# Performance work log

Hardware: AMD Instinct MI355X
Metric: run time of the kernel (lower is better)

Reference implementation:

```python
import jax, jax.numpy as jnp
import numpy as np

N, F_IN, HEADS, D_HEAD, NCLASS = 4096, 512, 8, 8, 16
NEG_INF = -9e15
LEAKY_SLOPE = 0.2


def setup_inputs() -> dict:
    key = jax.random.key(0)
    ks = jax.random.split(key, 8)
    x = jax.random.normal(ks[0], (N, F_IN), dtype=jnp.float32)
    adj = (jax.random.uniform(ks[1], (N, N)) < 0.01).astype(jnp.float32)
    adj = jnp.maximum(adj, jnp.eye(N, dtype=jnp.float32))
    s1 = 1.0 / np.sqrt(F_IN)
    s2 = 1.0 / np.sqrt(HEADS * D_HEAD)
    W1 = jax.random.normal(ks[2], (HEADS, F_IN, D_HEAD), dtype=jnp.float32) * s1
    a1_src = jax.random.normal(ks[3], (HEADS, D_HEAD), dtype=jnp.float32)
    a1_dst = jax.random.normal(ks[4], (HEADS, D_HEAD), dtype=jnp.float32)
    W2 = jax.random.normal(ks[5], (1, HEADS * D_HEAD, NCLASS), dtype=jnp.float32) * s2
    a2_src = jax.random.normal(ks[6], (1, NCLASS), dtype=jnp.float32)
    a2_dst = jax.random.normal(ks[7], (1, NCLASS), dtype=jnp.float32)
    return {"x": x, "adj": adj, "W1": W1, "a1_src": a1_src, "a1_dst": a1_dst,
            "W2": W2, "a2_src": a2_src, "a2_dst": a2_dst}


def gat_conv(x, adj, W, a_src, a_dst):
    # x: [N, F]; W: [H, F, D]; a_src/a_dst: [H, D]
    h = jnp.einsum('nf,hfd->hnd', x, W)              # [H, N, D]
    e_src = jnp.einsum('hnd,hd->hn', h, a_src)        # [H, N]
    e_dst = jnp.einsum('hnd,hd->hn', h, a_dst)        # [H, N]
    e = e_src[:, :, None] + e_dst[:, None, :]         # [H, N, N]
    e = jax.nn.leaky_relu(e, LEAKY_SLOPE)
    e = jnp.where(adj[None] > 0, e, NEG_INF)
    att = jax.nn.softmax(e, axis=-1)                  # masked row softmax
    out = jnp.einsum('hnm,hmd->hnd', att, h)          # [H, N, D]
    H, n, d = out.shape
    return jnp.transpose(out, (1, 0, 2)).reshape(n, H * d)  # concat heads


def reference(x, adj, W1, a1_src, a1_dst, W2, a2_src, a2_dst):
    # eval mode: dropout is identity
    h = gat_conv(x, adj, W1, a1_src, a1_dst)          # [N, 64]
    h = jax.nn.elu(h)
    out = gat_conv(h, adj, W2, a2_src, a2_dst)        # [N, NCLASS]
    return jax.nn.log_softmax(out, axis=-1)
```

## Files before the change

### kernel.cpp

```cpp
#include <hip/hip_runtime.h>
#include <math.h>

#define NN 4096
#define F_IN 512
#define HEADS 8
#define D_HEAD 8
#define C1 64
#define NCLASS 16
#define MAX_DEG 128
#define LEAKY 0.2f

__global__ __launch_bounds__(256) void k_wt(const float* __restrict__ W1,
                                            float* __restrict__ Wt) {
    const int i = blockIdx.x * 256 + threadIdx.x;
#pragma unroll
    for (int r = 0; r < 4; r++) {
        int o = r * 8192 + i;
        int c = o >> 9, f = o & 511;
        int h = c >> 3, d = c & 7;
        Wt[o] = W1[(h << 12) | (f << 3) | d];
    }
}

__global__ __launch_bounds__(256) void k_proj1(const float* __restrict__ x,
                                               const float* __restrict__ Wt,
                                               const float* __restrict__ a1s,
                                               const float* __restrict__ a1d,
                                               float* __restrict__ h1,
                                               float* __restrict__ es1,
                                               float* __restrict__ ed1) {
    __shared__ float xs[8 * F_IN];
    const int t = threadIdx.x;
    const int n0 = blockIdx.x * 8;
    const float4* x4 = (const float4*)(x + (size_t)n0 * F_IN);
    float4* xs4 = (float4*)xs;
#pragma unroll
    for (int i = 0; i < 4; i++) xs4[t + i * 256] = x4[t + i * 256];
    __syncthreads();

    const int c = t & 63;
    const int wv = t >> 6;
    const float4* wrow = (const float4*)(Wt + c * F_IN);
    const float4* r0 = (const float4*)(xs + (2 * wv + 0) * F_IN);
    const float4* r1 = (const float4*)(xs + (2 * wv + 1) * F_IN);
    float ax0 = 0.f, ay0 = 0.f, az0 = 0.f, aw0 = 0.f;
    float ax1 = 0.f, ay1 = 0.f, az1 = 0.f, aw1 = 0.f;
#pragma unroll 4
    for (int q = 0; q < F_IN / 4; q++) {
        float4 w = wrow[q];
        float4 u = r0[q];
        float4 v = r1[q];
        ax0 += u.x * w.x; ay0 += u.y * w.y; az0 += u.z * w.z; aw0 += u.w * w.w;
        ax1 += v.x * w.x; ay1 += v.y * w.y; az1 += v.z * w.z; aw1 += v.w * w.w;
    }
    float A = (ax0 + ay0) + (az0 + aw0);
    float B = (ax1 + ay1) + (az1 + aw1);
    const float as = a1s[c], ad = a1d[c];
    const int h = c >> 3, d = c & 7;
    float vals[2] = {A, B};
#pragma unroll
    for (int q = 0; q < 2; q++) {
        int n = n0 + 2 * wv + q;
        float v = vals[q];
        h1[(size_t)n * C1 + c] = v;
        float vs = v * as, vd = v * ad;
        vs += __shfl_xor(vs, 1, 64); vd += __shfl_xor(vd, 1, 64);
        vs += __shfl_xor(vs, 2, 64); vd += __shfl_xor(vd, 2, 64);
        vs += __shfl_xor(vs, 4, 64); vd += __shfl_xor(vd, 4, 64);
        if (d == 0) { es1[n * HEADS + h] = vs; ed1[n * HEADS + h] = vd; }
    }
}

__global__ __launch_bounds__(256) void k_csr(const float* __restrict__ adj,
                                             int* __restrict__ deg,
                                             int* __restrict__ cols) {
    __shared__ int cnt;
    __shared__ int cls[MAX_DEG];
    const int n = blockIdx.x, t = threadIdx.x;
    if (t == 0) cnt = 0;
    __syncthreads();
    const float4* row4 = (const float4*)(adj + (size_t)n * NN);
#pragma unroll
    for (int i = 0; i < 4; i++) {
        float4 v = row4[i * 256 + t];
        int base = (i * 256 + t) * 4;
        if (v.x > 0.f) { int p = atomicAdd(&cnt, 1); if (p < MAX_DEG) cls[p] = base; }
        if (v.y > 0.f) { int p = atomicAdd(&cnt, 1); if (p < MAX_DEG) cls[p] = base + 1; }
        if (v.z > 0.f) { int p = atomicAdd(&cnt, 1); if (p < MAX_DEG) cls[p] = base + 2; }
        if (v.w > 0.f) { int p = atomicAdd(&cnt, 1); if (p < MAX_DEG) cls[p] = base + 3; }
    }
    __syncthreads();
    int dc = cnt < MAX_DEG ? cnt : MAX_DEG;
    if (t == 0) deg[n] = dc;
    for (int i = t; i < dc; i += 256) cols[n * MAX_DEG + i] = cls[i];
}

__global__ __launch_bounds__(256) void k_layer1(const float* __restrict__ h1,
                                                const float* __restrict__ es1,
                                                const float* __restrict__ ed1,
                                                const int* __restrict__ deg,
                                                const int* __restrict__ cols,
                                                const float* __restrict__ W2,
                                                const float* __restrict__ a2s,
                                                const float* __restrict__ a2d,
                                                float* __restrict__ h2,
                                                float* __restrict__ es2,
                                                float* __restrict__ ed2) {
    __shared__ int cls[MAX_DEG];
    __shared__ float pM[4][C1], pS[4][C1], pA[4][C1];
    __shared__ float row[C1];
    const int n = blockIdx.x, t = threadIdx.x;
    const int wv = t >> 6, ln = t & 63;
    const int dg = deg[n];
    for (int i = t; i < dg; i += 256) cls[i] = cols[n * MAX_DEG + i];
    __syncthreads();
    const int h = ln >> 3;
    const float es = es1[n * HEADS + h];
    float M = -1e30f, S = 0.f, acc = 0.f;
    for (int j = wv; j < dg; j += 4) {
        int m = cls[j];
        float e = es + ed1[m * HEADS + h];
        e = e > 0.f ? e : LEAKY * e;
        float hv = h1[(size_t)m * C1 + ln];
        float Mn = fmaxf(M, e);
        float sc = __expf(M - Mn);
        float p = __expf(e - Mn);
        acc = acc * sc + p * hv;
        S = S * sc + p;
        M = Mn;
    }
    pM[wv][ln] = M; pS[wv][ln] = S; pA[wv][ln] = acc;
    __syncthreads();
    if (wv == 0) {
#pragma unroll
        for (int q = 1; q < 4; q++) {
            float Mo = pM[q][ln], So = pS[q][ln], ao = pA[q][ln];
            float Mn = fmaxf(M, Mo);
            float s1 = __expf(M - Mn), s2 = __expf(Mo - Mn);
            acc = acc * s1 + ao * s2;
            S = S * s1 + So * s2;
            M = Mn;
        }
        float o = acc / S;
        o = o > 0.f ? o : __expf(o) - 1.f;
        row[ln] = o;
    }
    __syncthreads();
    if (wv == 0) {
        const int k = ln & 15, g = ln >> 4;
        float hk = 0.f;
#pragma unroll
        for (int cc = 0; cc < 16; cc++) {
            int c2 = g * 16 + cc;
            hk += row[c2] * W2[c2 * NCLASS + k];
        }
        hk += __shfl_xor(hk, 16, 64);
        hk += __shfl_xor(hk, 32, 64);
        if (ln < 16) h2[n * NCLASS + k] = hk;
        float vs = hk * a2s[k];
        float vd = hk * a2d[k];
#pragma unroll
        for (int msk = 8; msk >= 1; msk >>= 1) {
            vs += __shfl_xor(vs, msk, 64);
            vd += __shfl_xor(vd, msk, 64);
        }
        if (ln == 0) { es2[n] = vs; ed2[n] = vd; }
    }
}

__global__ __launch_bounds__(64) void k_layer2(const float* __restrict__ h2,
                                               const float* __restrict__ es2,
                                               const float* __restrict__ ed2,
                                               const int* __restrict__ deg,
                                               const int* __restrict__ cols,
                                               float* __restrict__ out) {
    __shared__ int cls[MAX_DEG];
    const int n = blockIdx.x, t = threadIdx.x;
    const int dg = deg[n];
    for (int i = t; i < dg; i += 64) cls[i] = cols[n * MAX_DEG + i];
    __syncthreads();
    const int k = t & 15, g = t >> 4;
    const float es = es2[n];
    float M = -1e30f, S = 0.f, acc = 0.f;
    for (int j = g; j < dg; j += 4) {
        int m = cls[j];
        float e = es + ed2[m];
        e = e > 0.f ? e : LEAKY * e;
        float hv = h2[m * NCLASS + k];
        float Mn = fmaxf(M, e);
        float sc = __expf(M - Mn);
        float p = __expf(e - Mn);
        acc = acc * sc + p * hv;
        S = S * sc + p;
        M = Mn;
    }
#pragma unroll
    for (int msk = 16; msk <= 32; msk <<= 1) {
        float Mo = __shfl_xor(M, msk, 64);
        float So = __shfl_xor(S, msk, 64);
        float ao = __shfl_xor(acc, msk, 64);
        float Mn = fmaxf(M, Mo);
        float s1 = __expf(M - Mn), s2 = __expf(Mo - Mn);
        acc = acc * s1 + ao * s2;
        S = S * s1 + So * s2;
        M = Mn;
    }
    float v = acc / S;
    float mx = v;
#pragma unroll
    for (int msk = 1; msk <= 8; msk <<= 1) mx = fmaxf(mx, __shfl_xor(mx, msk, 64));
    float ex = __expf(v - mx);
    float se = ex;
#pragma unroll
    for (int msk = 1; msk <= 8; msk <<= 1) se += __shfl_xor(se, msk, 64);
    float r = v - mx - __logf(se);
    if (t < 16) out[n * NCLASS + k] = r;
}

extern "C" void kernel_launch(void* const* d_in, const int* in_sizes, int n_in,
                              void* d_out, int out_size, void* d_ws, size_t ws_size,
                              hipStream_t stream) {
    const float* x   = (const float*)d_in[0];
    const float* adj = (const float*)d_in[1];
    const float* W1  = (const float*)d_in[2];
    const float* a1s = (const float*)d_in[3];
    const float* a1d = (const float*)d_in[4];
    const float* W2  = (const float*)d_in[5];
    const float* a2s = (const float*)d_in[6];
    const float* a2d = (const float*)d_in[7];
    float* out = (float*)d_out;

    float* ws  = (float*)d_ws;
    float* h1  = ws;
    float* es1 = h1 + NN * C1;
    float* ed1 = es1 + NN * HEADS;
    float* h2  = ed1 + NN * HEADS;
    float* es2 = h2 + NN * NCLASS;
    float* ed2 = es2 + NN;
    int* deg  = (int*)(ed2 + NN);
    int* cols = deg + NN;
    float* Wt = (float*)(cols + NN * MAX_DEG);

    k_wt<<<32, 256, 0, stream>>>(W1, Wt);
    k_csr<<<NN, 256, 0, stream>>>(adj, deg, cols);
    k_proj1<<<NN / 8, 256, 0, stream>>>(x, Wt, a1s, a1d, h1, es1, ed1);
    k_layer1<<<NN, 256, 0, stream>>>(h1, es1, ed1, deg, cols, W2, a2s, a2d, h2, es2, ed2);
    k_layer2<<<NN, 64, 0, stream>>>(h2, es2, ed2, deg, cols, out);
}
```

Baseline: 161.8 us.

## Fuse all GAT stages into one persistent kernel with grid barriers

Replaces the five kernel launches (weight transpose, CSR build, projection, layer 1, layer 2) with a single kernel of 1024 blocks that processes 4 nodes per block and separates the stages with atomic-counter grid barriers. A tiny init kernel resets the barrier counters. The aim is to remove launch gaps and per-kernel tail effects. It relies on all 1024 blocks being co-resident (launch_bounds 256,4) to avoid deadlock. It also adds barrier spin latency and gives less parallelism per stage than one block per node.

```diff
diff --git a/kernel.cpp b/kernel.cpp
--- a/kernel.cpp
+++ b/kernel.cpp
@@ -9,212 +9,200 @@
 #define NCLASS 16
 #define MAX_DEG 128
 #define LEAKY 0.2f
-
-__global__ __launch_bounds__(256) void k_wt(const float* __restrict__ W1,
-                                            float* __restrict__ Wt) {
-    const int i = blockIdx.x * 256 + threadIdx.x;
-#pragma unroll
-    for (int r = 0; r < 4; r++) {
-        int o = r * 8192 + i;
-        int c = o >> 9, f = o & 511;
-        int h = c >> 3, d = c & 7;
-        Wt[o] = W1[(h << 12) | (f << 3) | d];
-    }
-}
-
-__global__ __launch_bounds__(256) void k_proj1(const float* __restrict__ x,
-                                               const float* __restrict__ Wt,
-                                               const float* __restrict__ a1s,
-                                               const float* __restrict__ a1d,
-                                               float* __restrict__ h1,
-                                               float* __restrict__ es1,
-                                               float* __restrict__ ed1) {
-    __shared__ float xs[8 * F_IN];
-    const int t = threadIdx.x;
-    const int n0 = blockIdx.x * 8;
-    const float4* x4 = (const float4*)(x + (size_t)n0 * F_IN);
-    float4* xs4 = (float4*)xs;
-#pragma unroll
-    for (int i = 0; i < 4; i++) xs4[t + i * 256] = x4[t + i * 256];
+#define NBLK 1024
+
+__device__ __forceinline__ void grid_barrier(int* bar) {
     __syncthreads();
-
-    const int c = t & 63;
-    const int wv = t >> 6;
-    const float4* wrow = (const float4*)(Wt + c * F_IN);
-    const float4* r0 = (const float4*)(xs + (2 * wv + 0) * F_IN);
-    const float4* r1 = (const float4*)(xs + (2 * wv + 1) * F_IN);
-    float ax0 = 0.f, ay0 = 0.f, az0 = 0.f, aw0 = 0.f;
-    float ax1 = 0.f, ay1 = 0.f, az1 = 0.f, aw1 = 0.f;
+    if (threadIdx.x == 0) {
+        __threadfence();
+        __hip_atomic_fetch_add(bar, 1, __ATOMIC_ACQ_REL, __HIP_MEMORY_SCOPE_AGENT);
+        while (__hip_atomic_load(bar, __ATOMIC_ACQUIRE, __HIP_MEMORY_SCOPE_AGENT) < NBLK)
+            __builtin_amdgcn_s_sleep(2);
+    }
+    __syncthreads();
+}
+
+__global__ __launch_bounds__(64) void k_init(int* __restrict__ bars) {
+    if (threadIdx.x < 8) bars[threadIdx.x] = 0;
+}
+
+__global__ __launch_bounds__(256, 4) void k_fused(
+    const float* __restrict__ x, const float* __restrict__ adj,
+    const float* __restrict__ W1, const float* __restrict__ a1s,
+    const float* __restrict__ a1d, const float* __restrict__ W2,
+    const float* __restrict__ a2s, const float* __restrict__ a2d,
+    float* __restrict__ out,
+    float* __restrict__ h1, float* __restrict__ es1, float* __restrict__ ed1,
+    float* __restrict__ h2, float* __restrict__ es2, float* __restrict__ ed2,
+    int* __restrict__ deg, int* __restrict__ cols, float* __restrict__ Wt,
+    int* __restrict__ bars) {
+    const int bid = blockIdx.x, t = threadIdx.x;
+    const int wv = t >> 6, ln = t & 63;
+
+    __shared__ int cnt;
+    __shared__ int cls[MAX_DEG];
+    __shared__ float xs[4 * F_IN];
+    __shared__ float pM[4][C1], pS[4][C1], pA[4][C1];
+    __shared__ float rowbuf[C1];
+
+    {
+        int idx = bid * 256 + t;
+        if (idx < C1 * F_IN) {
+            int c = idx >> 9, f = idx & 511;
+            Wt[idx] = W1[((c >> 3) << 12) | (f << 3) | (c & 7)];
+        }
+    }
+    for (int it = 0; it < 4; ++it) {
+        const int n = bid * 4 + it;
+        if (t == 0) cnt = 0;
+        __syncthreads();
+        const float4* row4 = (const float4*)(adj + (size_t)n * NN);
+#pragma unroll
+        for (int i = 0; i < 4; i++) {
+            float4 v = row4[i * 256 + t];
+            int base = (i * 256 + t) * 4;
+            if (v.x > 0.f) { int p = atomicAdd(&cnt, 1); if (p < MAX_DEG) cls[p] = base; }
+            if (v.y > 0.f) { int p = atomicAdd(&cnt, 1); if (p < MAX_DEG) cls[p] = base + 1; }
+            if (v.z > 0.f) { int p = atomicAdd(&cnt, 1); if (p < MAX_DEG) cls[p] = base + 2; }
+            if (v.w > 0.f) { int p = atomicAdd(&cnt, 1); if (p < MAX_DEG) cls[p] = base + 3; }
+        }
+        __syncthreads();
+        int dc = cnt < MAX_DEG ? cnt : MAX_DEG;
+        if (t == 0) deg[n] = dc;
+        for (int i = t; i < dc; i += 256) cols[n * MAX_DEG + i] = cls[i];
+        __syncthreads();
+    }
+    grid_barrier(&bars[0]);
+
+    {
+        const int n0 = bid * 4;
+        const float4* x4 = (const float4*)(x + (size_t)n0 * F_IN);
+        float4* xs4 = (float4*)xs;
+#pragma unroll
+        for (int i = 0; i < 2; i++) xs4[t + i * 256] = x4[t + i * 256];
+        __syncthreads();
+        const int c = ln;
+        const float4* wrow = (const float4*)(Wt + c * F_IN);
+        const float4* r0 = (const float4*)(xs + wv * F_IN);
+        float ax = 0.f, ay = 0.f, az = 0.f, aw = 0.f;
 #pragma unroll 4
-    for (int q = 0; q < F_IN / 4; q++) {
-        float4 w = wrow[q];
-        float4 u = r0[q];
-        float4 v = r1[q];
-        ax0 += u.x * w.x; ay0 += u.y * w.y; az0 += u.z * w.z; aw0 += u.w * w.w;
-        ax1 += v.x * w.x; ay1 += v.y * w.y; az1 += v.z * w.z; aw1 += v.w * w.w;
-    }
-    float A = (ax0 + ay0) + (az0 + aw0);
-    float B = (ax1 + ay1) + (az1 + aw1);
-    const float as = a1s[c], ad = a1d[c];
-    const int h = c >> 3, d = c & 7;
-    float vals[2] = {A, B};
-#pragma unroll
-    for (int q = 0; q < 2; q++) {
-        int n = n0 + 2 * wv + q;
-        float v = vals[q];
-        h1[(size_t)n * C1 + c] = v;
-        float vs = v * as, vd = v * ad;
+        for (int q = 0; q < F_IN / 4; q++) {
+            float4 w = wrow[q];
+            float4 u = r0[q];
+            ax += u.x * w.x; ay += u.y * w.y; az += u.z * w.z; aw += u.w * w.w;
+        }
+        float A = (ax + ay) + (az + aw);
+        const int n = n0 + wv;
+        h1[(size_t)n * C1 + c] = A;
+        float vs = A * a1s[c], vd = A * a1d[c];
         vs += __shfl_xor(vs, 1, 64); vd += __shfl_xor(vd, 1, 64);
         vs += __shfl_xor(vs, 2, 64); vd += __shfl_xor(vd, 2, 64);
         vs += __shfl_xor(vs, 4, 64); vd += __shfl_xor(vd, 4, 64);
-        if (d == 0) { es1[n * HEADS + h] = vs; ed1[n * HEADS + h] = vd; }
-    }
-}
-
-__global__ __launch_bounds__(256) void k_csr(const float* __restrict__ adj,
-                                             int* __restrict__ deg,
-                                             int* __restrict__ cols) {
-    __shared__ int cnt;
-    __shared__ int cls[MAX_DEG];
-    const int n = blockIdx.x, t = threadIdx.x;
-    if (t == 0) cnt = 0;
-    __syncthreads();
-    const float4* row4 = (const float4*)(adj + (size_t)n * NN);
-#pragma unroll
-    for (int i = 0; i < 4; i++) {
-        float4 v = row4[i * 256 + t];
-        int base = (i * 256 + t) * 4;
-        if (v.x > 0.f) { int p = atomicAdd(&cnt, 1); if (p < MAX_DEG) cls[p] = base; }
-        if (v.y > 0.f) { int p = atomicAdd(&cnt, 1); if (p < MAX_DEG) cls[p] = base + 1; }
-        if (v.z > 0.f) { int p = atomicAdd(&cnt, 1); if (p < MAX_DEG) cls[p] = base + 2; }
-        if (v.w > 0.f) { int p = atomicAdd(&cnt, 1); if (p < MAX_DEG) cls[p] = base + 3; }
-    }
-    __syncthreads();
-    int dc = cnt < MAX_DEG ? cnt : MAX_DEG;
-    if (t == 0) deg[n] = dc;
-    for (int i = t; i < dc; i += 256) cols[n * MAX_DEG + i] = cls[i];
-}
-
-__global__ __launch_bounds__(256) void k_layer1(const float* __restrict__ h1,
-                                                const float* __restrict__ es1,
-                                                const float* __restrict__ ed1,
-                                                const int* __restrict__ deg,
-                                                const int* __restrict__ cols,
-                                                const float* __restrict__ W2,
-                                                const float* __restrict__ a2s,
-                                                const float* __restrict__ a2d,
-                                                float* __restrict__ h2,
-                                                float* __restrict__ es2,
-                                                float* __restrict__ ed2) {
-    __shared__ int cls[MAX_DEG];
-    __shared__ float pM[4][C1], pS[4][C1], pA[4][C1];
-    __shared__ float row[C1];
-    const int n = blockIdx.x, t = threadIdx.x;
-    const int wv = t >> 6, ln = t & 63;
-    const int dg = deg[n];
-    for (int i = t; i < dg; i += 256) cls[i] = cols[n * MAX_DEG + i];
-    __syncthreads();
-    const int h = ln >> 3;
-    const float es = es1[n * HEADS + h];
-    float M = -1e30f, S = 0.f, acc = 0.f;
-    for (int j = wv; j < dg; j += 4) {
-        int m = cls[j];
-        float e = es + ed1[m * HEADS + h];
-        e = e > 0.f ? e : LEAKY * e;
-        float hv = h1[(size_t)m * C1 + ln];
-        float Mn = fmaxf(M, e);
-        float sc = __expf(M - Mn);
-        float p = __expf(e - Mn);
-        acc = acc * sc + p * hv;
-        S = S * sc + p;
-        M = Mn;
-    }
-    pM[wv][ln] = M; pS[wv][ln] = S; pA[wv][ln] = acc;
-    __syncthreads();
-    if (wv == 0) {
-#pragma unroll
-        for (int q = 1; q < 4; q++) {
-            float Mo = pM[q][ln], So = pS[q][ln], ao = pA[q][ln];
+        if ((c & 7) == 0) { es1[n * HEADS + (c >> 3)] = vs; ed1[n * HEADS + (c >> 3)] = vd; }
+    }
+    grid_barrier(&bars[1]);
+
+    for (int it = 0; it < 4; ++it) {
+        const int n = bid * 4 + it;
+        const int dg = deg[n];
+        for (int i = t; i < dg; i += 256) cls[i] = cols[n * MAX_DEG + i];
+        __syncthreads();
+        const int h = ln >> 3;
+        const float es = es1[n * HEADS + h];
+        float M = -1e30f, S = 0.f, acc = 0.f;
+        for (int j = wv; j < dg; j += 4) {
+            int m = cls[j];
+            float e = es + ed1[m * HEADS + h];
+            e = e > 0.f ? e : LEAKY * e;
+            float hv = h1[(size_t)m * C1 + ln];
+            float Mn = fmaxf(M, e);
+            float sc = __expf(M - Mn);
+            float p = __expf(e - Mn);
+            acc = acc * sc + p * hv;
+            S = S * sc + p;
+            M = Mn;
+        }
+        pM[wv][ln] = M; pS[wv][ln] = S; pA[wv][ln] = acc;
+        __syncthreads();
+        if (wv == 0) {
+#pragma unroll
+            for (int q = 1; q < 4; q++) {
+                float Mo = pM[q][ln], So = pS[q][ln], ao = pA[q][ln];
+                float Mn = fmaxf(M, Mo);
+                float s1 = __expf(M - Mn), s2 = __expf(Mo - Mn);
+                acc = acc * s1 + ao * s2;
+                S = S * s1 + So * s2;
+                M = Mn;
+            }
+            float o = acc / S;
+            o = o > 0.f ? o : __expf(o) - 1.f;
+            rowbuf[ln] = o;
+        }
+        __syncthreads();
+        if (wv == 0) {
+            const int k = ln & 15, g = ln >> 4;
+            float hk = 0.f;
+#pragma unroll
+            for (int cc = 0; cc < 16; cc++) {
+                int c2 = g * 16 + cc;
+                hk += rowbuf[c2] * W2[c2 * NCLASS + k];
+            }
+            hk += __shfl_xor(hk, 16, 64);
+            hk += __shfl_xor(hk, 32, 64);
+            if (ln < 16) h2[n * NCLASS + k] = hk;
+            float vs = hk * a2s[k];
+            float vd = hk * a2d[k];
+#pragma unroll
+            for (int msk = 8; msk >= 1; msk >>= 1) {
+                vs += __shfl_xor(vs, msk, 64);
+                vd += __shfl_xor(vd, msk, 64);
+            }
+            if (ln == 0) { es2[n] = vs; ed2[n] = vd; }
+        }
+        __syncthreads();
+    }
+    grid_barrier(&bars[2]);
+
+    {
+        const int n = bid * 4 + wv;
+        const int dg = deg[n];
+        const int k = ln & 15, g = ln >> 4;
+        const float es = es2[n];
+        float M = -1e30f, S = 0.f, acc = 0.f;
+        for (int j = g; j < dg; j += 4) {
+            int m = cols[n * MAX_DEG + j];
+            float e = es + ed2[m];
+            e = e > 0.f ? e : LEAKY * e;
+            float hv = h2[m * NCLASS + k];
+            float Mn = fmaxf(M, e);
+            float sc = __expf(M - Mn);
+            float p = __expf(e - Mn);
+            acc = acc * sc + p * hv;
+            S = S * sc + p;
+            M = Mn;
+        }
+#pragma unroll
+        for (int msk = 16; msk <= 32; msk <<= 1) {
+            float Mo = __shfl_xor(M, msk, 64);
+            float So = __shfl_xor(S, msk, 64);
+            float ao = __shfl_xor(acc, msk, 64);
             float Mn = fmaxf(M, Mo);
             float s1 = __expf(M - Mn), s2 = __expf(Mo - Mn);
             acc = acc * s1 + ao * s2;
             S = S * s1 + So * s2;
             M = Mn;
         }
-        float o = acc / S;
-        o = o > 0.f ? o : __expf(o) - 1.f;
-        row[ln] = o;
-    }
-    __syncthreads();
-    if (wv == 0) {
-        const int k = ln & 15, g = ln >> 4;
-        float hk = 0.f;
-#pragma unroll
-        for (int cc = 0; cc < 16; cc++) {
-            int c2 = g * 16 + cc;
-            hk += row[c2] * W2[c2 * NCLASS + k];
-        }
-        hk += __shfl_xor(hk, 16, 64);
-        hk += __shfl_xor(hk, 32, 64);
-        if (ln < 16) h2[n * NCLASS + k] = hk;
-        float vs = hk * a2s[k];
-        float vd = hk * a2d[k];
-#pragma unroll
-        for (int msk = 8; msk >= 1; msk >>= 1) {
-            vs += __shfl_xor(vs, msk, 64);
-            vd += __shfl_xor(vd, msk, 64);
-        }
-        if (ln == 0) { es2[n] = vs; ed2[n] = vd; }
-    }
-}
-
-__global__ __launch_bounds__(64) void k_layer2(const float* __restrict__ h2,
-                                               const float* __restrict__ es2,
-                                               const float* __restrict__ ed2,
-                                               const int* __restrict__ deg,
-                                               const int* __restrict__ cols,
-                                               float* __restrict__ out) {
-    __shared__ int cls[MAX_DEG];
-    const int n = blockIdx.x, t = threadIdx.x;
-    const int dg = deg[n];
-    for (int i = t; i < dg; i += 64) cls[i] = cols[n * MAX_DEG + i];
-    __syncthreads();
-    const int k = t & 15, g = t >> 4;
-    const float es = es2[n];
-    float M = -1e30f, S = 0.f, acc = 0.f;
-    for (int j = g; j < dg; j += 4) {
-        int m = cls[j];
-        float e = es + ed2[m];
-        e = e > 0.f ? e : LEAKY * e;
-        float hv = h2[m * NCLASS + k];
-        float Mn = fmaxf(M, e);
-        float sc = __expf(M - Mn);
-        float p = __expf(e - Mn);
-        acc = acc * sc + p * hv;
-        S = S * sc + p;
-        M = Mn;
-    }
-#pragma unroll
-    for (int msk = 16; msk <= 32; msk <<= 1) {
-        float Mo = __shfl_xor(M, msk, 64);
-        float So = __shfl_xor(S, msk, 64);
-        float ao = __shfl_xor(acc, msk, 64);
-        float Mn = fmaxf(M, Mo);
-        float s1 = __expf(M - Mn), s2 = __expf(Mo - Mn);
-        acc = acc * s1 + ao * s2;
-        S = S * s1 + So * s2;
-        M = Mn;
-    }
-    float v = acc / S;
-    float mx = v;
-#pragma unroll
-    for (int msk = 1; msk <= 8; msk <<= 1) mx = fmaxf(mx, __shfl_xor(mx, msk, 64));
-    float ex = __expf(v - mx);
-    float se = ex;
-#pragma unroll
-    for (int msk = 1; msk <= 8; msk <<= 1) se += __shfl_xor(se, msk, 64);
-    float r = v - mx - __logf(se);
-    if (t < 16) out[n * NCLASS + k] = r;
+        float v = acc / S;
+        float mx = v;
+#pragma unroll
+        for (int msk = 1; msk <= 8; msk <<= 1) mx = fmaxf(mx, __shfl_xor(mx, msk, 64));
+        float ex = __expf(v - mx);
+        float se = ex;
+#pragma unroll
+        for (int msk = 1; msk <= 8; msk <<= 1) se += __shfl_xor(se, msk, 64);
+        float r = v - mx - __logf(se);
+        if (ln < 16) out[n * NCLASS + k] = r;
+    }
 }
 
 extern "C" void kernel_launch(void* const* d_in, const int* in_sizes, int n_in,
@@ -240,10 +228,9 @@
     int* deg  = (int*)(ed2 + NN);
     int* cols = deg + NN;
     float* Wt = (float*)(cols + NN * MAX_DEG);
-
-    k_wt<<<32, 256, 0, stream>>>(W1, Wt);
-    k_csr<<<NN, 256, 0, stream>>>(adj, deg, cols);
-    k_proj1<<<NN / 8, 256, 0, stream>>>(x, Wt, a1s, a1d, h1, es1, ed1);
-    k_layer1<<<NN, 256, 0, stream>>>(h1, es1, ed1, deg, cols, W2, a2s, a2d, h2, es2, ed2);
-    k_layer2<<<NN, 64, 0, stream>>>(h2, es2, ed2, deg, cols, out);
-}
+    int* bars = (int*)(Wt + C1 * F_IN);
+
+    k_init<<<1, 64, 0, stream>>>(bars);
+    k_fused<<<NBLK, 256, 0, stream>>>(x, adj, W1, a1s, a1d, W2, a2s, a2d, out,
+                                      h1, es1, ed1, h2, es2, ed2, deg, cols, Wt, bars);
+}
```

Result: slower. 556.7 us (+244.2%).
